# Kernel tuning notes

Hardware: AMD Instinct MI355X
Metric: run time of the kernel (lower is better)

Reference implementation:

```python
import jax, jax.numpy as jnp
import numpy as np

P, R = 50000, 32        # num_patients, CP rank
N0, N1 = 2000, 1000     # modality sizes (e.g., diagnosis codes, drug codes)


def setup_inputs() -> dict:
    key = jax.random.key(0)
    k0, k1, k2 = jax.random.split(key, 3)
    return {
        "pt_reps": jax.random.uniform(k0, (P, R), dtype=jnp.float32),
        "U0": jax.random.uniform(k1, (N0, R), dtype=jnp.float32),
        "U1": jax.random.uniform(k2, (N1, R), dtype=jnp.float32),
    }


def reference(pt_reps, U0, U1):
    # torch.diag(U.sum(0)) chained matmuls == columnwise scale by product
    # of the other factors' column sums.
    s0 = U0.sum(axis=0)  # [R]
    s1 = U1.sum(axis=0)  # [R]
    # mode 0: pt_reps @ diag(s1) @ U0.T  -> [P, N0]
    V0 = (pt_reps * s1) @ U0.T
    # mode 1: pt_reps @ diag(s0) @ U1.T  -> [P, N1]
    V1 = (pt_reps * s0) @ U1.T
    return (V0, V1)
```

## Files before the change

kernel.cpp:

```cpp
#include <hip/hip_runtime.h>

#define R 32
#define PCHUNK 200

__global__ __launch_bounds__(1024) void colsum_kernel(
    const float* __restrict__ U0, int n0rows,
    const float* __restrict__ U1, int n1rows,
    float* __restrict__ ws)
{
    const float* U = (blockIdx.x == 0) ? U1 : U0;
    int rows       = (blockIdx.x == 0) ? n1rows : n0rows;
    float* out     = ws + blockIdx.x * R;

    int c = threadIdx.x & (R - 1);
    int g = threadIdx.x >> 5;

    float acc = 0.f;
    for (int r = g; r < rows; r += 32)
        acc += U[(size_t)r * R + c];

    __shared__ float red[32][R + 1];
    red[g][c] = acc;
    __syncthreads();
    for (int off = 16; off > 0; off >>= 1) {
        if (g < off) red[g][c] += red[g + off][c];
        __syncthreads();
    }
    if (g == 0) out[c] = red[0][c];
}

__global__ __launch_bounds__(256) void mode_kernel(
    const float* __restrict__ pt,
    const float* __restrict__ U,
    const float* __restrict__ s,
    float* __restrict__ V,
    int N, int P)
{
    const int lane = threadIdx.x & 63;
    const int wave = threadIdx.x >> 6;
    const int slot = (blockIdx.x * 4 + wave) * 64 + lane;
    const int nslots = N >> 1;
    const bool active = (slot < nslots);
    const int n0 = (active ? slot : 0) * 2;

    float ua[R], ub[R];
    {
        const float4* Ua = (const float4*)(U + (size_t)n0 * R);
        const float4* Ub = (const float4*)(U + (size_t)(n0 + 1) * R);
        const float4* S4 = (const float4*)s;
#pragma unroll
        for (int i = 0; i < R / 4; ++i) {
            float4 sv = S4[i];
            float4 x = Ua[i];
            float4 y = Ub[i];
            ua[4*i+0] = x.x * sv.x; ua[4*i+1] = x.y * sv.y;
            ua[4*i+2] = x.z * sv.z; ua[4*i+3] = x.w * sv.w;
            ub[4*i+0] = y.x * sv.x; ub[4*i+1] = y.y * sv.y;
            ub[4*i+2] = y.z * sv.z; ub[4*i+3] = y.w * sv.w;
        }
    }

    int p0 = blockIdx.y * PCHUNK;
    int p1 = min(p0 + PCHUNK, P);
    for (int p = p0; p < p1; ++p) {
        const float4* A4 = (const float4*)(pt + (size_t)p * R);
        float ax0 = 0.f, ax1 = 0.f, ay0 = 0.f, ay1 = 0.f;
#pragma unroll
        for (int i = 0; i < R / 4; ++i) {
            float4 a = A4[i];
            ax0 += a.x * ua[4*i+0] + a.y * ua[4*i+1];
            ax1 += a.z * ua[4*i+2] + a.w * ua[4*i+3];
            ay0 += a.x * ub[4*i+0] + a.y * ub[4*i+1];
            ay1 += a.z * ub[4*i+2] + a.w * ub[4*i+3];
        }
        if (active) {
            float2 v = make_float2(ax0 + ax1, ay0 + ay1);
            union { float2 f2; double d; } cvt;
            cvt.f2 = v;
            __builtin_nontemporal_store(cvt.d, (double*)(V + (size_t)p * N + n0));
        }
    }
}

extern "C" void kernel_launch(void* const* d_in, const int* in_sizes, int n_in,
                              void* d_out, int out_size, void* d_ws, size_t ws_size,
                              hipStream_t stream) {
    const float* pt = (const float*)d_in[0];
    const float* U0 = (const float*)d_in[1];
    const float* U1 = (const float*)d_in[2];
    int P  = in_sizes[0] / R;
    int N0 = in_sizes[1] / R;
    int N1 = in_sizes[2] / R;

    float* ws  = (float*)d_ws;
    float* out = (float*)d_out;

    colsum_kernel<<<dim3(2), dim3(1024), 0, stream>>>(U0, N0, U1, N1, ws);

    int gy  = (P + PCHUNK - 1) / PCHUNK;
    int gx0 = ((N0 / 2) + 255) / 256;
    int gx1 = ((N1 / 2) + 255) / 256;
    mode_kernel<<<dim3(gx0, gy), dim3(256), 0, stream>>>(pt, U0, ws, out, N0, P);
    mode_kernel<<<dim3(gx1, gy), dim3(256), 0, stream>>>(pt, U1, ws + R,
                                                         out + (size_t)P * N0, N1, P);
}
```

Measured before the change: 840.4 us.

## Fuse both mode kernels into one launch, halve row chunk, drop nontemporal stores

Merges the two per-mode launches into a single kernel whose column slots span both U0 and U1, so each block chooses its factor matrix and output region by slot index. The patient chunk per block is halved, which doubles the number of blocks along y. Output stores change from nontemporal double stores to plain float2 stores, and the output pointer is advanced incrementally instead of recomputed each row. This removes one launch and the tail imbalance between the two grids, at the cost of more blocks reloading their U rows and possible cache pollution from the 300MB of output writes.

```diff
diff --git a/kernel.cpp b/kernel.cpp
--- a/kernel.cpp
+++ b/kernel.cpp
@@ -1,7 +1,7 @@
 #include <hip/hip_runtime.h>
 
 #define R 32
-#define PCHUNK 200
+#define PCHUNK 100
 
 __global__ __launch_bounds__(1024) void colsum_kernel(
     const float* __restrict__ U0, int n0rows,
@@ -29,19 +29,28 @@
     if (g == 0) out[c] = red[0][c];
 }
 
-__global__ __launch_bounds__(256) void mode_kernel(
+__global__ __launch_bounds__(256) void fused_mode_kernel(
     const float* __restrict__ pt,
-    const float* __restrict__ U,
-    const float* __restrict__ s,
-    float* __restrict__ V,
-    int N, int P)
+    const float* __restrict__ U0,
+    const float* __restrict__ U1,
+    const float* __restrict__ ws,
+    float* __restrict__ out,
+    int N0, int N1, int P)
 {
     const int lane = threadIdx.x & 63;
     const int wave = threadIdx.x >> 6;
     const int slot = (blockIdx.x * 4 + wave) * 64 + lane;
-    const int nslots = N >> 1;
-    const bool active = (slot < nslots);
-    const int n0 = (active ? slot : 0) * 2;
+    const int slots0 = N0 >> 1;
+    const int slots1 = N1 >> 1;
+    const bool active = (slot < slots0 + slots1);
+    const bool is0 = (slot < slots0);
+
+    const float* U = is0 ? U0 : U1;
+    const float* s = is0 ? ws : ws + R;
+    const int    N = is0 ? N0 : N1;
+    float*       V = is0 ? out : out + (size_t)P * N0;
+    const int   sl = active ? (is0 ? slot : slot - slots0) : 0;
+    const int   n0 = sl * 2;
 
     float ua[R], ub[R];
     {
@@ -60,9 +69,10 @@
         }
     }
 
+    float* vptr = V + (size_t)blockIdx.y * PCHUNK * N + n0;
     int p0 = blockIdx.y * PCHUNK;
     int p1 = min(p0 + PCHUNK, P);
-    for (int p = p0; p < p1; ++p) {
+    for (int p = p0; p < p1; ++p, vptr += N) {
         const float4* A4 = (const float4*)(pt + (size_t)p * R);
         float ax0 = 0.f, ax1 = 0.f, ay0 = 0.f, ay1 = 0.f;
 #pragma unroll
@@ -74,10 +84,7 @@
             ay1 += a.z * ub[4*i+2] + a.w * ub[4*i+3];
         }
         if (active) {
-            float2 v = make_float2(ax0 + ax1, ay0 + ay1);
-            union { float2 f2; double d; } cvt;
-            cvt.f2 = v;
-            __builtin_nontemporal_store(cvt.d, (double*)(V + (size_t)p * N + n0));
+            *(float2*)vptr = make_float2(ax0 + ax1, ay0 + ay1);
         }
     }
 }
@@ -97,10 +104,9 @@
 
     colsum_kernel<<<dim3(2), dim3(1024), 0, stream>>>(U0, N0, U1, N1, ws);
 
-    int gy  = (P + PCHUNK - 1) / PCHUNK;
-    int gx0 = ((N0 / 2) + 255) / 256;
-    int gx1 = ((N1 / 2) + 255) / 256;
-    mode_kernel<<<dim3(gx0, gy), dim3(256), 0, stream>>>(pt, U0, ws, out, N0, P);
-    mode_kernel<<<dim3(gx1, gy), dim3(256), 0, stream>>>(pt, U1, ws + R,
-                                                         out + (size_t)P * N0, N1, P);
+    int total_slots = (N0 >> 1) + (N1 >> 1);
+    int gx = (total_slots + 255) / 256;
+    int gy = (P + PCHUNK - 1) / PCHUNK;
+    fused_mode_kernel<<<dim3(gx, gy), dim3(256), 0, stream>>>(
+        pt, U0, U1, ws, out, N0, N1, P);
 }
```

Measured after the change: 845.7 us. Within noise of the previous version (+0.6%).
